# Performance work log

Hardware: AMD Instinct MI355X
Metric: run time of the kernel (lower is better)

## Reference

```python
import jax, jax.numpy as jnp
import numpy as np
from jax import lax


def setup_inputs() -> dict:
    key = jax.random.key(0)
    k1, k2 = jax.random.split(key)
    B, H, W, C = 8, 32, 32, 512
    N = 16384
    feature_batch = jax.random.normal(k1, (B, H, W, C), dtype=jnp.float32)
    mb = jax.random.normal(k2, (N, C), dtype=jnp.float32)
    return {"feature_batch": feature_batch, "mb": mb, "b": 9}


def reference(feature_batch, mb, b):
    B, H, W, C = feature_batch.shape
    fv = feature_batch.reshape(B * H * W, C)                       # (Q, C)
    sq = (
        jnp.sum(fv * fv, axis=1)[:, None]
        + jnp.sum(mb * mb, axis=1)[None, :]
        - 2.0 * (fv @ mb.T)
    )                                                               # (Q, N)
    sq = jnp.maximum(sq, 0.0)  # guard fp round-off before sqrt
    # smallest-b distances, sorted ascending (top_k of negated values)
    neg_topk = lax.top_k(-sq, b)[0]                                 # (Q, b)
    top_k_dists_squared = -neg_topk
    pixel_scores = jnp.sqrt(top_k_dists_squared[:, 0]).reshape(B, H * W)
    max_idx = jnp.argmax(pixel_scores, axis=1)                      # (B,)
    softmax_args = jnp.sqrt(
        top_k_dists_squared.reshape(B, H * W, b)[jnp.arange(B), max_idx, :]
    )                                                               # (B, b)
    image_scores = softmax_args[:, 0]
    if b > 1:
        image_scores = image_scores * (1.0 - jax.nn.softmax(softmax_args, axis=1)[:, 0])
    pixel_scores = pixel_scores.reshape(B, 1, H, W)
    return pixel_scores, image_scores
```

## Files before the change

kernel.cpp:

```cpp
#include <hip/hip_runtime.h>
#include <hip/hip_bf16.h>

typedef unsigned short u16;

#define M_ROWS 8192
#define N_ROWS 16384
#define KDIM   512
#define BM     128
#define BN     128
#define BK     64
#define NCHUNKS 16
#define NPER   (N_ROWS / NCHUNKS)
#define TOPK   9

typedef __attribute__((ext_vector_type(8)))  short bf16x8;
typedef __attribute__((ext_vector_type(16))) float f32x16;

__device__ __forceinline__ void gload_lds16(const void* g, void* l) {
  __builtin_amdgcn_global_load_lds(
      (const __attribute__((address_space(1))) void*)g,
      (__attribute__((address_space(3))) void*)l,
      16, 0, 0);
}

__device__ __forceinline__ u16 f2bf(float x) {
  union { float f; unsigned u; } c; c.f = x;
  unsigned u = c.u;
  u += 0x7fffu + ((u >> 16) & 1u);
  return (u16)(u >> 16);
}

__device__ __forceinline__ void topk_update(float v, float best[TOPK]) {
  if (v < best[TOPK - 1]) {
    #pragma unroll
    for (int i = 0; i < TOPK; ++i) {
      float b = best[i];
      best[i] = fminf(b, v);
      v = fmaxf(b, v);
    }
  }
}

__global__ __launch_bounds__(256) void prep_kernel(
    const float* __restrict__ fv, const float* __restrict__ mb,
    u16* __restrict__ fvb, u16* __restrict__ mbb,
    float* __restrict__ nf, float* __restrict__ nm_perm)
{
  int idx = blockIdx.x * 4 + (threadIdx.x >> 6);
  int l = threadIdx.x & 63;
  const float* src; u16* dst;
  if (idx < M_ROWS) {
    src = fv + (size_t)idx * KDIM; dst = fvb + (size_t)idx * KDIM;
  } else {
    int r = idx - M_ROWS;
    src = mb + (size_t)r * KDIM; dst = mbb + (size_t)r * KDIM;
  }
  float4 x0 = ((const float4*)src)[2 * l];
  float4 x1 = ((const float4*)src)[2 * l + 1];
  float s = x0.x * x0.x + x0.y * x0.y + x0.z * x0.z + x0.w * x0.w
          + x1.x * x1.x + x1.y * x1.y + x1.z * x1.z + x1.w * x1.w;
  uint4 o;
  o.x = (unsigned)f2bf(x0.x) | ((unsigned)f2bf(x0.y) << 16);
  o.y = (unsigned)f2bf(x0.z) | ((unsigned)f2bf(x0.w) << 16);
  o.z = (unsigned)f2bf(x1.x) | ((unsigned)f2bf(x1.y) << 16);
  o.w = (unsigned)f2bf(x1.z) | ((unsigned)f2bf(x1.w) << 16);
  ((uint4*)dst)[l] = o;
  #pragma unroll
  for (int off = 32; off > 0; off >>= 1) s += __shfl_down(s, off, 64);
  if (l == 0) {
    if (idx < M_ROWS) {
      nf[idx] = s;
    } else {
      int n  = idx - M_ROWS;
      int ig = n >> 5;
      int w5 = n & 31;
      int h  = (w5 >> 2) & 1;
      int r  = (w5 & 3) | ((w5 >> 3) << 2);
      nm_perm[(ig * 2 + h) * 16 + r] = s;
    }
  }
}

__global__ __launch_bounds__(256) void gemm_topk_kernel(
    const u16* __restrict__ fvb, const u16* __restrict__ mbb,
    const float* __restrict__ nm_perm, float* __restrict__ partial)
{
  __shared__ __align__(16) u16 As[BM * BK];
  __shared__ __align__(16) u16 Bs[BN * BK];

  const int t   = threadIdx.x;
  const int l   = t & 63;
  const int w   = t >> 6;
  const int h   = l >> 5;
  const int c31 = l & 31;
  const int cx  = c31 & 7;

  const int m0    = blockIdx.x * BM;
  const int ncoff = blockIdx.y * NPER;

  const int srow_lo = l >> 3;
  const int sc      = ((l & 7) ^ srow_lo) * 8;

  float best[TOPK];
  #pragma unroll
  for (int i = 0; i < TOPK; ++i) best[i] = 3.4e38f;
  float T = 3.4e38f;

  for (int nt = 0; nt < NPER / BN; ++nt) {
    const int nbase = ncoff + nt * BN;
    f32x16 acc[4];
    #pragma unroll
    for (int i = 0; i < 4; ++i)
      #pragma unroll
      for (int r = 0; r < 16; ++r) acc[i][r] = 0.0f;

    for (int kc = 0; kc < KDIM / BK; ++kc) {
      __syncthreads();
      const int kb = kc * BK + sc;
      #pragma unroll
      for (int i = 0; i < 4; ++i) {
        gload_lds16(fvb + (size_t)(m0 + w * 32 + i * 8 + srow_lo) * KDIM + kb,
                    &As[(w * 32 + i * 8) * BK]);
        gload_lds16(mbb + (size_t)(nbase + w * 32 + i * 8 + srow_lo) * KDIM + kb,
                    &Bs[(w * 32 + i * 8) * BK]);
      }
      __syncthreads();
      #pragma unroll
      for (int kk = 0; kk < 4; ++kk) {
        const int ch = ((kk * 2 + h) ^ cx) * 8;
        bf16x8 fvf = *(const bf16x8*)&As[(w * 32 + c31) * BK + ch];
        #pragma unroll
        for (int i = 0; i < 4; ++i) {
          bf16x8 mbf = *(const bf16x8*)&Bs[(i * 32 + c31) * BK + ch];
          acc[i] = __builtin_amdgcn_mfma_f32_32x32x16_bf16(mbf, fvf, acc[i], 0, 0, 0);
        }
      }
    }

    #pragma unroll
    for (int i = 0; i < 4; ++i) {
      const float4* np = (const float4*)&nm_perm[(((nbase >> 5) + i) * 2 + h) * 16];
      float v[16];
      float bmin = 3.4e38f;
      #pragma unroll
      for (int rr = 0; rr < 4; ++rr) {
        float4 q = np[rr];
        v[rr * 4 + 0] = fmaf(-2.0f, acc[i][rr * 4 + 0], q.x);
        v[rr * 4 + 1] = fmaf(-2.0f, acc[i][rr * 4 + 1], q.y);
        v[rr * 4 + 2] = fmaf(-2.0f, acc[i][rr * 4 + 2], q.z);
        v[rr * 4 + 3] = fmaf(-2.0f, acc[i][rr * 4 + 3], q.w);
      }
      #pragma unroll
      for (int r = 0; r < 16; ++r) bmin = fminf(bmin, v[r]);
      if (bmin < T) {
        #pragma unroll
        for (int r = 0; r < 16; ++r) topk_update(v[r], best);
      }
    }
    T = fminf(best[TOPK - 1], __shfl_xor(best[TOPK - 1], 32, 64));
  }

  {
    float tmp[TOPK];
    #pragma unroll
    for (int s = 0; s < TOPK; ++s) tmp[s] = __shfl_xor(best[s], 32, 64);
    #pragma unroll
    for (int s = 0; s < TOPK; ++s) topk_update(tmp[s], best);
  }
  int m = m0 + w * 32 + c31;
  size_t base = ((size_t)blockIdx.y * M_ROWS + m) * TOPK;
  if (h == 0) {
    #pragma unroll
    for (int s = 0; s < 5; ++s) partial[base + s] = best[s];
  } else {
    #pragma unroll
    for (int s = 5; s < TOPK; ++s) partial[base + s] = best[s];
  }
}

__global__ __launch_bounds__(256) void merge_kernel(
    const float* __restrict__ partial, const float* __restrict__ nf,
    float* __restrict__ final9, float* __restrict__ out_pix)
{
  int row = blockIdx.x * 256 + threadIdx.x;
  float best[TOPK];
  #pragma unroll
  for (int i = 0; i < TOPK; ++i) best[i] = 3.4e38f;
  for (int s = 0; s < NCHUNKS; ++s) {
    const float* p = &partial[((size_t)s * M_ROWS + row) * TOPK];
    #pragma unroll
    for (int i = 0; i < TOPK; ++i) topk_update(p[i], best);
  }
  float nfr = nf[row];
  float d[TOPK];
  #pragma unroll
  for (int i = 0; i < TOPK; ++i) d[i] = sqrtf(fmaxf(best[i] + nfr, 0.0f));
  out_pix[row] = d[0];
  #pragma unroll
  for (int i = 0; i < TOPK; ++i) final9[(size_t)row * TOPK + i] = d[i];
}

__global__ __launch_bounds__(256) void img_kernel(
    const float* __restrict__ out_pix, const float* __restrict__ final9,
    const int* __restrict__ bptr, float* __restrict__ out_img)
{
  int img = blockIdx.x, t = threadIdx.x;
  float bv = -1.0f; int bi = 0;
  for (int p = t; p < 1024; p += 256) {
    float v = out_pix[img * 1024 + p];
    if (v > bv) { bv = v; bi = p; }
  }
  __shared__ float sv[256];
  __shared__ int   si[256];
  sv[t] = bv; si[t] = bi;
  __syncthreads();
  for (int off = 128; off > 0; off >>= 1) {
    if (t < off) {
      float v2 = sv[t + off]; int i2 = si[t + off];
      if (v2 > sv[t] || (v2 == sv[t] && i2 < si[t])) { sv[t] = v2; si[t] = i2; }
    }
    __syncthreads();
  }
  if (t == 0) {
    int row = img * 1024 + si[0];
    int b = bptr[0];
    float s0 = final9[(size_t)row * TOPK + 0];
    float score = s0;
    if (b > 1) {
      int bb = b < TOPK ? b : TOPK;
      float mx = s0;
      for (int i = 1; i < bb; ++i) mx = fmaxf(mx, final9[(size_t)row * TOPK + i]);
      float den = 0.0f;
      for (int i = 0; i < bb; ++i) den += expf(final9[(size_t)row * TOPK + i] - mx);
      score = s0 * (1.0f - expf(s0 - mx) / den);
    }
    out_img[img] = score;
  }
}

extern "C" void kernel_launch(void* const* d_in, const int* in_sizes, int n_in,
                              void* d_out, int out_size, void* d_ws, size_t ws_size,
                              hipStream_t stream) {
  const float* fv   = (const float*)d_in[0];
  const float* mb   = (const float*)d_in[1];
  const int*   bptr = (const int*)d_in[2];
  float* out = (float*)d_out;

  char* w = (char*)d_ws;
  u16*   fvb     = (u16*)w;
  u16*   mbb     = (u16*)(w + 8388608);
  float* nf      = (float*)(w + 25165824);
  float* nm_perm = (float*)(w + 25198592);
  float* partial = (float*)(w + 25264128);
  float* final9  = (float*)(w + 29982720);

  hipLaunchKernelGGL(prep_kernel, dim3((M_ROWS + N_ROWS) / 4), dim3(256), 0, stream,
                     fv, mb, fvb, mbb, nf, nm_perm);
  hipLaunchKernelGGL(gemm_topk_kernel, dim3(M_ROWS / BM, NCHUNKS), dim3(256), 0, stream,
                     fvb, mbb, nm_perm, partial);
  hipLaunchKernelGGL(merge_kernel, dim3(M_ROWS / 256), dim3(256), 0, stream,
                     partial, nf, final9, out);
  hipLaunchKernelGGL(img_kernel, dim3(8), dim3(256), 0, stream,
                     out, final9, bptr, out + M_ROWS);
}
```

Before: 342.4 us.

## Double-buffer LDS tiles and use a 2x2 warp layout in the GEMM-topk kernel

Adds double-buffered shared memory for the A and B tiles, so global-to-LDS loads of the next K-chunk (and of the next N-tile) are issued before computing the current one, and one barrier per step is removed. Changes the warp tiling from 1x4 (each warp owns 32 rows against all 128 columns) to 2x2 (64 rows by 64 columns per warp), which lowers LDS fragment reads per MFMA. Each warp now keeps two top-k lists and writes partial results per column half, so NCHUNKS is halved while the merge reads 2*NCHUNKS partial slices. This trades higher register and LDS use for better latency hiding and less LDS traffic, and the grid now has half as many blocks.

```diff
diff --git a/kernel.cpp b/kernel.cpp
--- a/kernel.cpp
+++ b/kernel.cpp
@@ -9,8 +9,9 @@
 #define BM     128
 #define BN     128
 #define BK     64
-#define NCHUNKS 16
+#define NCHUNKS 8
 #define NPER   (N_ROWS / NCHUNKS)
+#define NT_CNT (NPER / BN)
 #define TOPK   9
 
 typedef __attribute__((ext_vector_type(8)))  short bf16x8;
@@ -85,12 +86,14 @@
     const u16* __restrict__ fvb, const u16* __restrict__ mbb,
     const float* __restrict__ nm_perm, float* __restrict__ partial)
 {
-  __shared__ __align__(16) u16 As[BM * BK];
-  __shared__ __align__(16) u16 Bs[BN * BK];
+  __shared__ __align__(16) u16 As[2][BM * BK];
+  __shared__ __align__(16) u16 Bs[2][BN * BK];
 
   const int t   = threadIdx.x;
   const int l   = t & 63;
   const int w   = t >> 6;
+  const int wm  = w & 1;
+  const int wn  = w >> 1;
   const int h   = l >> 5;
   const int c31 = l & 31;
   const int cx  = c31 & 7;
@@ -101,80 +104,119 @@
   const int srow_lo = l >> 3;
   const int sc      = ((l & 7) ^ srow_lo) * 8;
 
-  float best[TOPK];
-  #pragma unroll
-  for (int i = 0; i < TOPK; ++i) best[i] = 3.4e38f;
-  float T = 3.4e38f;
-
-  for (int nt = 0; nt < NPER / BN; ++nt) {
+  float best[2][TOPK];
+  float T[2];
+  #pragma unroll
+  for (int j = 0; j < 2; ++j) {
+    T[j] = 3.4e38f;
+    #pragma unroll
+    for (int i = 0; i < TOPK; ++i) best[j][i] = 3.4e38f;
+  }
+
+  {
+    const int kb = sc;
+    #pragma unroll
+    for (int i = 0; i < 4; ++i) {
+      gload_lds16(fvb + (size_t)(m0 + w * 32 + i * 8 + srow_lo) * KDIM + kb,
+                  &As[0][(w * 32 + i * 8) * BK]);
+      gload_lds16(mbb + (size_t)(ncoff + w * 32 + i * 8 + srow_lo) * KDIM + kb,
+                  &Bs[0][(w * 32 + i * 8) * BK]);
+    }
+  }
+
+  for (int nt = 0; nt < NT_CNT; ++nt) {
     const int nbase = ncoff + nt * BN;
-    f32x16 acc[4];
-    #pragma unroll
-    for (int i = 0; i < 4; ++i)
-      #pragma unroll
-      for (int r = 0; r < 16; ++r) acc[i][r] = 0.0f;
+    f32x16 acc[2][2];
+    #pragma unroll
+    for (int i = 0; i < 2; ++i)
+      #pragma unroll
+      for (int j = 0; j < 2; ++j)
+        #pragma unroll
+        for (int r = 0; r < 16; ++r) acc[i][j][r] = 0.0f;
 
     for (int kc = 0; kc < KDIM / BK; ++kc) {
+      const int cur = kc & 1;
       __syncthreads();
-      const int kb = kc * BK + sc;
-      #pragma unroll
-      for (int i = 0; i < 4; ++i) {
-        gload_lds16(fvb + (size_t)(m0 + w * 32 + i * 8 + srow_lo) * KDIM + kb,
-                    &As[(w * 32 + i * 8) * BK]);
-        gload_lds16(mbb + (size_t)(nbase + w * 32 + i * 8 + srow_lo) * KDIM + kb,
-                    &Bs[(w * 32 + i * 8) * BK]);
+      if (kc < KDIM / BK - 1) {
+        const int kb = (kc + 1) * BK + sc;
+        #pragma unroll
+        for (int i = 0; i < 4; ++i) {
+          gload_lds16(fvb + (size_t)(m0 + w * 32 + i * 8 + srow_lo) * KDIM + kb,
+                      &As[cur ^ 1][(w * 32 + i * 8) * BK]);
+          gload_lds16(mbb + (size_t)(nbase + w * 32 + i * 8 + srow_lo) * KDIM + kb,
+                      &Bs[cur ^ 1][(w * 32 + i * 8) * BK]);
+        }
+      } else if (nt + 1 < NT_CNT) {
+        const int kb = sc;
+        #pragma unroll
+        for (int i = 0; i < 4; ++i) {
+          gload_lds16(fvb + (size_t)(m0 + w * 32 + i * 8 + srow_lo) * KDIM + kb,
+                      &As[cur ^ 1][(w * 32 + i * 8) * BK]);
+          gload_lds16(mbb + (size_t)(nbase + BN + w * 32 + i * 8 + srow_lo) * KDIM + kb,
+                      &Bs[cur ^ 1][(w * 32 + i * 8) * BK]);
+        }
       }
-      __syncthreads();
       #pragma unroll
       for (int kk = 0; kk < 4; ++kk) {
         const int ch = ((kk * 2 + h) ^ cx) * 8;
-        bf16x8 fvf = *(const bf16x8*)&As[(w * 32 + c31) * BK + ch];
-        #pragma unroll
-        for (int i = 0; i < 4; ++i) {
-          bf16x8 mbf = *(const bf16x8*)&Bs[(i * 32 + c31) * BK + ch];
-          acc[i] = __builtin_amdgcn_mfma_f32_32x32x16_bf16(mbf, fvf, acc[i], 0, 0, 0);
+        bf16x8 fvf0 = *(const bf16x8*)&As[cur][(wm * 64 + c31) * BK + ch];
+        bf16x8 fvf1 = *(const bf16x8*)&As[cur][(wm * 64 + 32 + c31) * BK + ch];
+        bf16x8 mbf0 = *(const bf16x8*)&Bs[cur][(wn * 64 + c31) * BK + ch];
+        bf16x8 mbf1 = *(const bf16x8*)&Bs[cur][(wn * 64 + 32 + c31) * BK + ch];
+        acc[0][0] = __builtin_amdgcn_mfma_f32_32x32x16_bf16(mbf0, fvf0, acc[0][0], 0, 0, 0);
+        acc[0][1] = __builtin_amdgcn_mfma_f32_32x32x16_bf16(mbf0, fvf1, acc[0][1], 0, 0, 0);
+        acc[1][0] = __builtin_amdgcn_mfma_f32_32x32x16_bf16(mbf1, fvf0, acc[1][0], 0, 0, 0);
+        acc[1][1] = __builtin_amdgcn_mfma_f32_32x32x16_bf16(mbf1, fvf1, acc[1][1], 0, 0, 0);
+      }
+    }
+
+    #pragma unroll
+    for (int j = 0; j < 2; ++j) {
+      float v[32];
+      float bmin = 3.4e38f;
+      #pragma unroll
+      for (int i = 0; i < 2; ++i) {
+        const float4* np =
+            (const float4*)&nm_perm[((((nbase >> 5) + wn * 2 + i)) * 2 + h) * 16];
+        #pragma unroll
+        for (int rr = 0; rr < 4; ++rr) {
+          float4 q = np[rr];
+          v[i * 16 + rr * 4 + 0] = fmaf(-2.0f, acc[i][j][rr * 4 + 0], q.x);
+          v[i * 16 + rr * 4 + 1] = fmaf(-2.0f, acc[i][j][rr * 4 + 1], q.y);
+          v[i * 16 + rr * 4 + 2] = fmaf(-2.0f, acc[i][j][rr * 4 + 2], q.z);
+          v[i * 16 + rr * 4 + 3] = fmaf(-2.0f, acc[i][j][rr * 4 + 3], q.w);
         }
       }
-    }
-
-    #pragma unroll
-    for (int i = 0; i < 4; ++i) {
-      const float4* np = (const float4*)&nm_perm[(((nbase >> 5) + i) * 2 + h) * 16];
-      float v[16];
-      float bmin = 3.4e38f;
-      #pragma unroll
-      for (int rr = 0; rr < 4; ++rr) {
-        float4 q = np[rr];
-        v[rr * 4 + 0] = fmaf(-2.0f, acc[i][rr * 4 + 0], q.x);
-        v[rr * 4 + 1] = fmaf(-2.0f, acc[i][rr * 4 + 1], q.y);
-        v[rr * 4 + 2] = fmaf(-2.0f, acc[i][rr * 4 + 2], q.z);
-        v[rr * 4 + 3] = fmaf(-2.0f, acc[i][rr * 4 + 3], q.w);
+      #pragma unroll
+      for (int r = 0; r < 32; ++r) bmin = fminf(bmin, v[r]);
+      if (bmin < T[j]) {
+        #pragma unroll
+        for (int r = 0; r < 32; ++r) topk_update(v[r], best[j]);
       }
-      #pragma unroll
-      for (int r = 0; r < 16; ++r) bmin = fminf(bmin, v[r]);
-      if (bmin < T) {
-        #pragma unroll
-        for (int r = 0; r < 16; ++r) topk_update(v[r], best);
-      }
-    }
-    T = fminf(best[TOPK - 1], __shfl_xor(best[TOPK - 1], 32, 64));
-  }
-
-  {
+      float th = best[j][TOPK - 1];
+      T[j] = fminf(th, __shfl_xor(th, 32, 64));
+    }
+  }
+
+  #pragma unroll
+  for (int j = 0; j < 2; ++j) {
     float tmp[TOPK];
     #pragma unroll
-    for (int s = 0; s < TOPK; ++s) tmp[s] = __shfl_xor(best[s], 32, 64);
-    #pragma unroll
-    for (int s = 0; s < TOPK; ++s) topk_update(tmp[s], best);
-  }
-  int m = m0 + w * 32 + c31;
-  size_t base = ((size_t)blockIdx.y * M_ROWS + m) * TOPK;
-  if (h == 0) {
-    #pragma unroll
-    for (int s = 0; s < 5; ++s) partial[base + s] = best[s];
-  } else {
-    #pragma unroll
-    for (int s = 5; s < TOPK; ++s) partial[base + s] = best[s];
+    for (int s = 0; s < TOPK; ++s) tmp[s] = __shfl_xor(best[j][s], 32, 64);
+    #pragma unroll
+    for (int s = 0; s < TOPK; ++s) topk_update(tmp[s], best[j]);
+  }
+  #pragma unroll
+  for (int j = 0; j < 2; ++j) {
+    int m = m0 + wm * 64 + j * 32 + c31;
+    size_t base = ((size_t)(blockIdx.y * 2 + wn) * M_ROWS + m) * TOPK;
+    if (h == 0) {
+      #pragma unroll
+      for (int s = 0; s < 5; ++s) partial[base + s] = best[j][s];
+    } else {
+      #pragma unroll
+      for (int s = 5; s < TOPK; ++s) partial[base + s] = best[j][s];
+    }
   }
 }
 
@@ -186,7 +228,7 @@
   float best[TOPK];
   #pragma unroll
   for (int i = 0; i < TOPK; ++i) best[i] = 3.4e38f;
-  for (int s = 0; s < NCHUNKS; ++s) {
+  for (int s = 0; s < 2 * NCHUNKS; ++s) {
     const float* p = &partial[((size_t)s * M_ROWS + row) * TOPK];
     #pragma unroll
     for (int i = 0; i < TOPK; ++i) topk_update(p[i], best);
```

After: 317.7 us. -7.2%, faster.
